# Optimization experiments

Hardware: AMD Instinct MI355X
Metric: run time of the kernel (lower is better)

The kernel has to match this reference:

```python
import jax, jax.numpy as jnp
import numpy as np

N = 50000      # nodes
E = 800000     # edges (before self-loops)
C_IN, C_H, C_OUT = 128, 64, 64
NEG_SLOPE = 0.2  # PyG GATConv default LeakyReLU slope


def setup_inputs() -> dict:
    key = jax.random.key(0)
    ks = jax.random.split(key, 16)
    def w(k, shape, fan_in):
        return jax.random.normal(k, shape, jnp.float32) / np.sqrt(fan_in)
    return {
        "x": jax.random.normal(ks[0], (N, C_IN), jnp.float32),
        "edge_index": jax.random.randint(ks[1], (2, E), 0, N, jnp.int32),
        "W1": w(ks[2], (C_IN, C_H), C_IN),
        "a_src1": w(ks[3], (C_H,), C_H),
        "a_dst1": w(ks[4], (C_H,), C_H),
        "b1": jnp.zeros((C_H,), jnp.float32),
        "W2": w(ks[5], (C_H, C_H), C_H),
        "a_src2": w(ks[6], (C_H,), C_H),
        "a_dst2": w(ks[7], (C_H,), C_H),
        "b2": jnp.zeros((C_H,), jnp.float32),
        "W3": w(ks[8], (C_H, C_OUT), C_H),
        "a_src3": w(ks[9], (C_OUT,), C_OUT),
        "a_dst3": w(ks[10], (C_OUT,), C_OUT),
        "b3": jnp.zeros((C_OUT,), jnp.float32),
    }


def _gat_conv(x, src, dst, W, a_src, a_dst, b):
    # Single-head GATConv (eval mode, self-loops already appended).
    h = x @ W                                   # [N, C]
    alpha_s = h @ a_src                         # [N]
    alpha_d = h @ a_dst                         # [N]
    e = jax.nn.leaky_relu(alpha_s[src] + alpha_d[dst], NEG_SLOPE)  # [E']
    # segment softmax over edges sharing the same destination node
    m = jax.lax.stop_gradient(jax.ops.segment_max(e, dst, num_segments=N))
    w = jnp.exp(e - m[dst])
    denom = jax.ops.segment_sum(w, dst, num_segments=N)
    alpha = w / denom[dst]                      # [E']
    out = jax.ops.segment_sum(h[src] * alpha[:, None], dst, num_segments=N)
    return out + b


def reference(x, edge_index, W1, a_src1, a_dst1, b1, W2, a_src2, a_dst2, b2,
              W3, a_src3, a_dst3, b3):
    loop = jnp.arange(N, dtype=edge_index.dtype)
    src = jnp.concatenate([edge_index[0], loop])  # add self-loops (PyG default)
    dst = jnp.concatenate([edge_index[1], loop])
    h = jax.nn.elu(_gat_conv(x, src, dst, W1, a_src1, a_dst1, b1))
    h = jax.nn.elu(_gat_conv(h, src, dst, W2, a_src2, a_dst2, b2))
    return _gat_conv(h, src, dst, W3, a_src3, a_dst3, b3)
```

## Files before the change

kernel.cpp:

```cpp
#include <hip/hip_runtime.h>
#include <hip/hip_bf16.h>
#include <math.h>

#define N_NODES 50000
#define N_EDGES 800000
#define ET_EDGES (N_EDGES + N_NODES)
#define NEG_SLOPE 0.2f
#define NBUCK ((N_NODES + 255) / 256)
#define CHUNK 4096
#define CAP   8192
#define BIN_GRID ((ET_EDGES + CHUNK - 1) / CHUNK)
#define GEMM_GRID ((N_NODES + 63) / 64)

typedef __hip_bfloat16 bf16;
typedef float f32x2 __attribute__((ext_vector_type(2)));

__device__ inline float bfbits(unsigned short u) {
    return __uint_as_float(((unsigned)u) << 16);
}
__device__ inline float bflo(unsigned u) { return __uint_as_float(u << 16); }
__device__ inline float bfhi(unsigned u) { return __uint_as_float(u & 0xffff0000u); }
__device__ inline f32x2 unpk(unsigned u) {
    f32x2 r; r.x = bflo(u); r.y = bfhi(u); return r;
}
__device__ inline f32x2 bcast2(float v) { f32x2 r; r.x = v; r.y = v; return r; }

struct PrepArgs {
    const void* src[12];
    float*      dst[12];
    int         n[12];
};

__global__ __launch_bounds__(256)
void prep(PrepArgs a, const unsigned short* __restrict__ w1raw,
          unsigned* __restrict__ flag, int* __restrict__ cur256)
{
    __shared__ unsigned sflag;
    const int tid = threadIdx.x;
    if (tid < 64) {
        float v0 = bfbits(w1raw[2 * tid]);
        float v1 = bfbits(w1raw[2 * tid + 1]);
        bool bad = !(fabsf(v0) <= 64.f && fabsf(v1) <= 64.f);
        unsigned long long b = __ballot(bad);
        if (tid == 0) sflag = (b == 0ull) ? 1u : 0u;
    }
    __syncthreads();
    const bool isbf = (sflag != 0u);
    const int which = blockIdx.y;

    if (which == 12) {
        int i = blockIdx.x * 256 + tid;
        if (i < NBUCK) cur256[i] = i * CAP;
        if (blockIdx.x == 0 && tid == 0) *flag = isbf ? 1u : 0u;
        return;
    }
    const int n = a.n[which];
    const void* s = a.src[which];
    float* d = a.dst[which];
    for (int i = blockIdx.x * 256 + tid; i < n; i += 8 * 256)
        d[i] = isbf ? bfbits(((const unsigned short*)s)[i])
                    : ((const float*)s)[i];
}

__device__ void binpass_body(unsigned char* smem, int bid,
                             const int* __restrict__ ei,
                             int* __restrict__ cur256,
                             unsigned* __restrict__ scratch)
{
    int* hist   = (int*)smem;
    int* lpre   = hist + NBUCK;
    int* lcur   = lpre + NBUCK + 1;
    int* gbase  = lcur + NBUCK;
    int* scan_a = gbase + NBUCK;
    unsigned* entry = (unsigned*)(scan_a + 256);

    const int tid = threadIdx.x;
    const int e0  = bid * CHUNK;
    const int n   = min(CHUNK, ET_EDGES - e0);

    if (tid < NBUCK) hist[tid] = 0;
    __syncthreads();

    for (int k = tid; k < n; k += 256) {
        int e = e0 + k;
        int d = (e < N_EDGES) ? ei[N_EDGES + e] : e - N_EDGES;
        atomicAdd(&hist[d >> 8], 1);
    }
    __syncthreads();

    int v = (tid < NBUCK) ? hist[tid] : 0;
    scan_a[tid] = v;
    __syncthreads();
    for (int off = 1; off < 256; off <<= 1) {
        int t = (tid >= off) ? scan_a[tid - off] : 0;
        __syncthreads();
        scan_a[tid] += t;
        __syncthreads();
    }
    if (tid < NBUCK) lpre[tid] = scan_a[tid] - v;
    if (tid == NBUCK - 1) lpre[NBUCK] = scan_a[tid];
    if (tid < NBUCK) {
        gbase[tid] = v ? atomicAdd(&cur256[tid], v) : 0;
        lcur[tid] = 0;
    }
    __syncthreads();

    for (int k = tid; k < n; k += 256) {
        int e = e0 + k;
        int s, d;
        if (e < N_EDGES) { s = ei[e]; d = ei[N_EDGES + e]; }
        else             { s = d = e - N_EDGES; }
        int b = d >> 8;
        int p = atomicAdd(&lcur[b], 1);
        entry[lpre[b] + p] = ((unsigned)s << 8) | (unsigned)(d & 255);
    }
    __syncthreads();

    for (int i = tid; i < n; i += 256) {
        int lo = 0, hi = NBUCK;
        while (hi - lo > 1) {
            int mid = (lo + hi) >> 1;
            if (lpre[mid] <= i) lo = mid; else hi = mid;
        }
        scratch[gbase[lo] + (i - lpre[lo])] = entry[i];
    }
}

__global__ __launch_bounds__(256)
void fine_scatter(const int* __restrict__ cur256,
                  const unsigned* __restrict__ scratch,
                  int* __restrict__ csr_src,
                  int* __restrict__ rowptr)
{
    __shared__ int scnt[256];
    __shared__ int cnt[256];
    __shared__ int pre[256];
    const int tid = threadIdx.x;
    const int b   = blockIdx.x;
    const int nb  = b * 256;
    const int nn  = min(256, N_NODES - nb);

    int bv = (tid < NBUCK) ? (cur256[tid] - tid * CAP) : 0;
    scnt[tid] = bv;
    __syncthreads();
    for (int off = 1; off < 256; off <<= 1) {
        int u = (tid >= off) ? scnt[tid - off] : 0;
        __syncthreads();
        scnt[tid] += u;
        __syncthreads();
    }
    const int gb = scnt[b] - (cur256[b] - b * CAP);
    const int n  = cur256[b] - b * CAP;
    const long seg = (long)b * CAP;

    cnt[tid] = 0;
    __syncthreads();
    for (int i = tid; i < n; i += 256)
        atomicAdd(&cnt[scratch[seg + i] & 255u], 1);
    __syncthreads();

    int v = cnt[tid];
    pre[tid] = v;
    __syncthreads();
    for (int off = 1; off < 256; off <<= 1) {
        int t = (tid >= off) ? pre[tid - off] : 0;
        __syncthreads();
        pre[tid] += t;
        __syncthreads();
    }
    int excl = pre[tid] - v + gb;
    if (tid < nn) rowptr[nb + tid] = excl;
    if (b == NBUCK - 1 && tid == 0) rowptr[N_NODES] = ET_EDGES;
    cnt[tid] = excl;
    __syncthreads();

    for (int i = tid; i < n; i += 256) {
        unsigned e = scratch[seg + i];
        int p = atomicAdd(&cnt[e & 255u], 1);
        csr_src[p] = (int)(e >> 8);
    }
}

template<int CIN, int XMODE>
__device__ void gemm_body(unsigned char* smem, int bid,
                          const void* __restrict__ x,
                          const float* __restrict__ W,
                          const float* __restrict__ a_src,
                          const float* __restrict__ a_dst,
                          const unsigned* __restrict__ flag,
                          bf16* __restrict__ hb,
                          float* __restrict__ as_out,
                          float* __restrict__ ad_out)
{
    constexpr int CINP = CIN + 4;
    float* sW = (float*)smem;
    float* sx = sW + CIN * 64;
    const bool isbf = (XMODE == 2) || (XMODE == 1 && *flag != 0u);
    const int tid  = threadIdx.x;
    const int colg = tid & 15;
    const int rowg = tid >> 4;
    const int c0   = colg * 4;
    const int r0l  = rowg * 4;
    const int row0 = bid * 64;

    for (int i = tid * 4; i < CIN * 64; i += 1024)
        *(float4*)&sW[i] = *(const float4*)&W[i];

    const long xbase = (long)row0 * CIN;
    const int  tile  = 64 * CIN;
    const int  limit = (N_NODES - row0) * CIN;
    if (isbf) {
        const unsigned short* xb = (const unsigned short*)x + xbase;
        for (int i = tid * 4; i < tile; i += 1024) {
            float4 v = {0.f, 0.f, 0.f, 0.f};
            if (i < limit) {
                ushort4 u = *(const ushort4*)&xb[i];
                v.x = bfbits(u.x); v.y = bfbits(u.y);
                v.z = bfbits(u.z); v.w = bfbits(u.w);
            }
            const int r = i / CIN, k = i & (CIN - 1);
            *(float4*)&sx[r * CINP + k] = v;
        }
    } else {
        const float* xf = (const float*)x + xbase;
        for (int i = tid * 4; i < tile; i += 1024) {
            float4 v = {0.f, 0.f, 0.f, 0.f};
            if (i < limit) v = *(const float4*)&xf[i];
            const int r = i / CIN, k = i & (CIN - 1);
            *(float4*)&sx[r * CINP + k] = v;
        }
    }
    __syncthreads();

    f32x2 acc[4][2];
#pragma unroll
    for (int r = 0; r < 4; ++r) {
        acc[r][0] = (f32x2){0.f, 0.f};
        acc[r][1] = (f32x2){0.f, 0.f};
    }

#pragma unroll 2
    for (int kk = 0; kk < CIN; kk += 4) {
        const float4 w0 = *(const float4*)&sW[(kk + 0) * 64 + c0];
        const float4 w1 = *(const float4*)&sW[(kk + 1) * 64 + c0];
        const float4 w2 = *(const float4*)&sW[(kk + 2) * 64 + c0];
        const float4 w3 = *(const float4*)&sW[(kk + 3) * 64 + c0];
        f32x2 w0lo; w0lo.x = w0.x; w0lo.y = w0.y;
        f32x2 w0hi; w0hi.x = w0.z; w0hi.y = w0.w;
        f32x2 w1lo; w1lo.x = w1.x; w1lo.y = w1.y;
        f32x2 w1hi; w1hi.x = w1.z; w1hi.y = w1.w;
        f32x2 w2lo; w2lo.x = w2.x; w2lo.y = w2.y;
        f32x2 w2hi; w2hi.x = w2.z; w2hi.y = w2.w;
        f32x2 w3lo; w3lo.x = w3.x; w3lo.y = w3.y;
        f32x2 w3hi; w3hi.x = w3.z; w3hi.y = w3.w;
#pragma unroll
        for (int r = 0; r < 4; ++r) {
            const float4 xv = *(const float4*)&sx[(r0l + r) * CINP + kk];
            acc[r][0] = __builtin_elementwise_fma(bcast2(xv.x), w0lo, acc[r][0]);
            acc[r][1] = __builtin_elementwise_fma(bcast2(xv.x), w0hi, acc[r][1]);
            acc[r][0] = __builtin_elementwise_fma(bcast2(xv.y), w1lo, acc[r][0]);
            acc[r][1] = __builtin_elementwise_fma(bcast2(xv.y), w1hi, acc[r][1]);
            acc[r][0] = __builtin_elementwise_fma(bcast2(xv.z), w2lo, acc[r][0]);
            acc[r][1] = __builtin_elementwise_fma(bcast2(xv.z), w2hi, acc[r][1]);
            acc[r][0] = __builtin_elementwise_fma(bcast2(xv.w), w3lo, acc[r][0]);
            acc[r][1] = __builtin_elementwise_fma(bcast2(xv.w), w3hi, acc[r][1]);
        }
    }

    const float4 sa4 = *(const float4*)&a_src[c0];
    const float4 sd4 = *(const float4*)&a_dst[c0];
#pragma unroll
    for (int r = 0; r < 4; ++r) {
        const int row = row0 + r0l + r;
        const float h0 = acc[r][0].x, h1 = acc[r][0].y;
        const float h2 = acc[r][1].x, h3 = acc[r][1].y;
        float vs = fmaf(h0, sa4.x, fmaf(h1, sa4.y, fmaf(h2, sa4.z, h3 * sa4.w)));
        float vd = fmaf(h0, sd4.x, fmaf(h1, sd4.y, fmaf(h2, sd4.z, h3 * sd4.w)));
#pragma unroll
        for (int off = 1; off < 16; off <<= 1) {
            vs += __shfl_xor(vs, off, 64);
            vd += __shfl_xor(vd, off, 64);
        }
        if (row < N_NODES) {
            uint2 u;
            u.x = ((unsigned)__bfloat16_as_ushort(__float2bfloat16(h0))) |
                  (((unsigned)__bfloat16_as_ushort(__float2bfloat16(h1))) << 16);
            u.y = ((unsigned)__bfloat16_as_ushort(__float2bfloat16(h2))) |
                  (((unsigned)__bfloat16_as_ushort(__float2bfloat16(h3))) << 16);
            *(uint2*)&((unsigned short*)hb)[(long)row * 64 + c0] = u;
            if (colg == 0) { as_out[row] = vs; ad_out[row] = vd; }
        }
    }
}

template<int CIN, int XMODE>
__global__ __launch_bounds__(256)
void gemm_alpha(const void* __restrict__ x, const float* __restrict__ W,
                const float* __restrict__ a_src, const float* __restrict__ a_dst,
                const unsigned* __restrict__ flag, bf16* __restrict__ hb,
                float* __restrict__ as_out, float* __restrict__ ad_out)
{
    __shared__ __align__(16) unsigned char smem[(CIN * 64 + 64 * (CIN + 4)) * 4];
    gemm_body<CIN, XMODE>(smem, blockIdx.x, x, W, a_src, a_dst, flag, hb, as_out, ad_out);
}

__global__ __launch_bounds__(256)
void gemm1_bin(const void* __restrict__ x, const float* __restrict__ W,
               const float* __restrict__ a_src, const float* __restrict__ a_dst,
               const unsigned* __restrict__ flag, bf16* __restrict__ hb,
               float* __restrict__ as_out, float* __restrict__ ad_out,
               const int* __restrict__ ei, int* __restrict__ cur256,
               unsigned* __restrict__ scratch)
{
    __shared__ __align__(16) unsigned char smem[(128 * 64 + 64 * 132) * 4];
    if (blockIdx.x < BIN_GRID)
        binpass_body(smem, blockIdx.x, ei, cur256, scratch);
    else
        gemm_body<128, 1>(smem, blockIdx.x - BIN_GRID, x, W, a_src, a_dst,
                          flag, hb, as_out, ad_out);
}

#define EDGE4_FMA(wX, pX) {                                                  \
    f32x2 w2_ = { wX, wX };                                                  \
    A0 = __builtin_elementwise_fma(w2_, unpk(pX.x), A0);                     \
    A1 = __builtin_elementwise_fma(w2_, unpk(pX.y), A1);                     \
    A2 = __builtin_elementwise_fma(w2_, unpk(pX.z), A2);                     \
    A3 = __builtin_elementwise_fma(w2_, unpk(pX.w), A3); }

template<bool DO_ELU, int OMODE>
__global__ __launch_bounds__(256)
void gat_gather(const int* __restrict__ rowptr,
                const int* __restrict__ csr_src,
                const float* __restrict__ as_in,
                const float* __restrict__ ad_in,
                const unsigned short* __restrict__ hb_in,
                const float* __restrict__ bias,
                void* __restrict__ out,
                const unsigned* __restrict__ flag)
{
    __shared__ int2 s_sw[16 * 64];
    const int tid  = threadIdx.x;
    const int lane = tid & 63;
    const int l16  = lane & 15;
    const int sub  = l16 >> 3;
    const int c8   = (l16 & 7) * 8;
    const int grp  = tid >> 4;
    const int node = blockIdx.x * 16 + grp;

    const int beg = rowptr[node];
    const int deg = rowptr[node + 1] - beg;
    const float adv = ad_in[node];
    const int nst = (deg < 64) ? deg : 64;

    for (int j = l16; j < nst; j += 16) {
        int s = csr_src[beg + j];
        float v = as_in[s] + adv;
        v = (v > 0.f) ? v : NEG_SLOPE * v;
        s_sw[grp * 64 + j] = make_int2(s, __float_as_int(__expf(fminf(v, 60.f))));
    }

    f32x2 A0 = {0.f, 0.f}, A1 = {0.f, 0.f}, A2 = {0.f, 0.f}, A3 = {0.f, 0.f};
    float dsum = 0.f;

    for (int j0 = 0; j0 < deg; j0 += 8) {
        const int jA = j0 + sub,     jB = j0 + 2 + sub;
        const int jC = j0 + 4 + sub, jD = j0 + 6 + sub;
        const bool vA = jA < deg, vB = jB < deg, vC = jC < deg, vD = jD < deg;
        int sA = 0, sB = 0, sC = 0, sD = 0;
        float wA = 0.f, wB = 0.f, wC = 0.f, wD = 0.f;
        if (vA) {
            if (jA < 64) { int2 t = s_sw[grp * 64 + jA]; sA = t.x; wA = __int_as_float(t.y); }
            else { sA = csr_src[beg + jA]; float v = as_in[sA] + adv;
                   v = (v > 0.f) ? v : NEG_SLOPE * v; wA = __expf(fminf(v, 60.f)); }
        }
        if (vB) {
            if (jB < 64) { int2 t = s_sw[grp * 64 + jB]; sB = t.x; wB = __int_as_float(t.y); }
            else { sB = csr_src[beg + jB]; float v = as_in[sB] + adv;
                   v = (v > 0.f) ? v : NEG_SLOPE * v; wB = __expf(fminf(v, 60.f)); }
        }
        if (vC) {
            if (jC < 64) { int2 t = s_sw[grp * 64 + jC]; sC = t.x; wC = __int_as_float(t.y); }
            else { sC = csr_src[beg + jC]; float v = as_in[sC] + adv;
                   v = (v > 0.f) ? v : NEG_SLOPE * v; wC = __expf(fminf(v, 60.f)); }
        }
        if (vD) {
            if (jD < 64) { int2 t = s_sw[grp * 64 + jD]; sD = t.x; wD = __int_as_float(t.y); }
            else { sD = csr_src[beg + jD]; float v = as_in[sD] + adv;
                   v = (v > 0.f) ? v : NEG_SLOPE * v; wD = __expf(fminf(v, 60.f)); }
        }
        uint4 pA={0u,0u,0u,0u}, pB={0u,0u,0u,0u}, pC={0u,0u,0u,0u}, pD={0u,0u,0u,0u};
        if (vA) pA = *(const uint4*)&hb_in[(long)sA * 64 + c8];
        if (vB) pB = *(const uint4*)&hb_in[(long)sB * 64 + c8];
        if (vC) pC = *(const uint4*)&hb_in[(long)sC * 64 + c8];
        if (vD) pD = *(const uint4*)&hb_in[(long)sD * 64 + c8];
        EDGE4_FMA(wA, pA) EDGE4_FMA(wB, pB) EDGE4_FMA(wC, pC) EDGE4_FMA(wD, pD)
        dsum += (wA + wB) + (wC + wD);
    }

    float a0 = A0.x, a1 = A0.y, a2 = A1.x, a3 = A1.y;
    float a4 = A2.x, a5 = A2.y, a6 = A3.x, a7 = A3.y;
    a0 += __shfl_xor(a0, 8, 64); a1 += __shfl_xor(a1, 8, 64);
    a2 += __shfl_xor(a2, 8, 64); a3 += __shfl_xor(a3, 8, 64);
    a4 += __shfl_xor(a4, 8, 64); a5 += __shfl_xor(a5, 8, 64);
    a6 += __shfl_xor(a6, 8, 64); a7 += __shfl_xor(a7, 8, 64);
    dsum += __shfl_xor(dsum, 8, 64);

    if (sub == 0) {
        float inv = 1.f / dsum;
        float r[8] = {a0, a1, a2, a3, a4, a5, a6, a7};
#pragma unroll
        for (int k = 0; k < 8; ++k) {
            r[k] = r[k] * inv + bias[c8 + k];
            if (DO_ELU) r[k] = (r[k] > 0.f) ? r[k] : expm1f(r[k]);
        }
        long o = (long)node * 64 + c8;
        bool bfst = (OMODE == 0) || (*flag != 0u);
        if (bfst) {
            uint4 u;
            u.x = ((unsigned)__bfloat16_as_ushort(__float2bfloat16(r[0]))) |
                  (((unsigned)__bfloat16_as_ushort(__float2bfloat16(r[1]))) << 16);
            u.y = ((unsigned)__bfloat16_as_ushort(__float2bfloat16(r[2]))) |
                  (((unsigned)__bfloat16_as_ushort(__float2bfloat16(r[3]))) << 16);
            u.z = ((unsigned)__bfloat16_as_ushort(__float2bfloat16(r[4]))) |
                  (((unsigned)__bfloat16_as_ushort(__float2bfloat16(r[5]))) << 16);
            u.w = ((unsigned)__bfloat16_as_ushort(__float2bfloat16(r[6]))) |
                  (((unsigned)__bfloat16_as_ushort(__float2bfloat16(r[7]))) << 16);
            *(uint4*)&((unsigned short*)out)[o] = u;
        } else {
            float4 f0 = {r[0], r[1], r[2], r[3]};
            float4 f1 = {r[4], r[5], r[6], r[7]};
            *(float4*)&((float*)out)[o]     = f0;
            *(float4*)&((float*)out)[o + 4] = f1;
        }
    }
}

extern "C" void kernel_launch(void* const* d_in, const int* in_sizes, int n_in,
                              void* d_out, int out_size, void* d_ws, size_t ws_size,
                              hipStream_t stream)
{
    const void* x  = d_in[0];
    const int*  ei = (const int*)d_in[1];
    const void* pW1 = d_in[2],  *pas1 = d_in[3],  *pad1 = d_in[4],  *pb1 = d_in[5];
    const void* pW2 = d_in[6],  *pas2 = d_in[7],  *pad2 = d_in[8],  *pb2 = d_in[9];
    const void* pW3 = d_in[10], *pas3 = d_in[11], *pad3 = d_in[12], *pb3 = d_in[13];

    float* ws = (float*)d_ws;
    bf16*     hbA    = (bf16*)ws;
    bf16*     hbB    = (bf16*)(ws + (long)N_NODES * 32);
    float*    as_    = ws + (long)N_NODES * 64;
    float*    ad_    = as_ + N_NODES;
    int*      cur256 = (int*)(ad_ + N_NODES);
    int*      rowptr = cur256 + NBUCK;
    int*      csr_src= rowptr + N_NODES + 1;
    unsigned* scratch= (unsigned*)(csr_src + ET_EDGES);
    float*    prm    = (float*)(scratch + (long)NBUCK * CAP);
    unsigned* flag   = (unsigned*)(prm + 20000);

    float* W1 = prm;     float* as1 = W1 + 8192; float* ad1 = as1 + 64; float* b1 = ad1 + 64;
    float* W2 = b1 + 64; float* as2 = W2 + 4096; float* ad2 = as2 + 64; float* b2 = ad2 + 64;
    float* W3 = b2 + 64; float* as3 = W3 + 4096; float* ad3 = as3 + 64; float* b3 = ad3 + 64;

    PrepArgs pa;
    const void* srcs[12] = {pW1, pas1, pad1, pb1, pW2, pas2, pad2, pb2, pW3, pas3, pad3, pb3};
    float*      dsts[12] = {W1, as1, ad1, b1, W2, as2, ad2, b2, W3, as3, ad3, b3};
    int         ns[12]   = {8192, 64, 64, 64, 4096, 64, 64, 64, 4096, 64, 64, 64};
    for (int i = 0; i < 12; ++i) { pa.src[i] = srcs[i]; pa.dst[i] = dsts[i]; pa.n[i] = ns[i]; }
    prep<<<dim3(8, 13), 256, 0, stream>>>(pa, (const unsigned short*)pW1, flag, cur256);

    const int gat_grid = (N_NODES + 15) / 16;

    gemm1_bin<<<BIN_GRID + GEMM_GRID, 256, 0, stream>>>(
        x, W1, as1, ad1, flag, hbA, as_, ad_, ei, cur256, scratch);
    fine_scatter<<<NBUCK, 256, 0, stream>>>(cur256, scratch, csr_src, rowptr);
    gat_gather<true, 0><<<gat_grid, 256, 0, stream>>>(
        rowptr, csr_src, as_, ad_, (const unsigned short*)hbA, b1, hbB, flag);

    gemm_alpha<64, 2><<<GEMM_GRID, 256, 0, stream>>>(
        hbB, W2, as2, ad2, flag, hbA, as_, ad_);
    gat_gather<true, 0><<<gat_grid, 256, 0, stream>>>(
        rowptr, csr_src, as_, ad_, (const unsigned short*)hbA, b2, hbB, flag);

    gemm_alpha<64, 2><<<GEMM_GRID, 256, 0, stream>>>(
        hbB, W3, as3, ad3, flag, hbA, as_, ad_);
    gat_gather<false, 1><<<gat_grid, 256, 0, stream>>>(
        rowptr, csr_src, as_, ad_, (const unsigned short*)hbA, b3, d_out, flag);
}
```

Measured before the change: 234.4 us.

## Fuse all GAT stages into one persistent kernel with grid barriers

Replaces the seven separate launches (bin+gemm1, fine scatter, three gathers, two gemms) with one persistent kernel of 768 blocks that loops over each stage's work items and separates stages with a software grid barrier on global atomics. The GEMM is restructured to stage K in 64-wide chunks so shared memory fits within a smaller fixed buffer, allowing 3 blocks per CU. This targets launch gaps and inter-kernel idle time. The risks are barrier spin cost, deadlock if not all 768 blocks are co-resident, and lower per-stage occupancy.

```diff
diff --git a/kernel.cpp b/kernel.cpp
--- a/kernel.cpp
+++ b/kernel.cpp
@@ -11,6 +11,8 @@
 #define CAP   8192
 #define BIN_GRID ((ET_EDGES + CHUNK - 1) / CHUNK)
 #define GEMM_GRID ((N_NODES + 63) / 64)
+#define GAT_GRID (N_NODES / 16)
+#define MEGA_GRID 768
 
 typedef __hip_bfloat16 bf16;
 typedef float f32x2 __attribute__((ext_vector_type(2)));
@@ -33,7 +35,8 @@
 
 __global__ __launch_bounds__(256)
 void prep(PrepArgs a, const unsigned short* __restrict__ w1raw,
-          unsigned* __restrict__ flag, int* __restrict__ cur256)
+          unsigned* __restrict__ flag, int* __restrict__ cur256,
+          int* __restrict__ bar)
 {
     __shared__ unsigned sflag;
     const int tid = threadIdx.x;
@@ -51,7 +54,11 @@
     if (which == 12) {
         int i = blockIdx.x * 256 + tid;
         if (i < NBUCK) cur256[i] = i * CAP;
-        if (blockIdx.x == 0 && tid == 0) *flag = isbf ? 1u : 0u;
+        if (blockIdx.x == 0 && tid == 0) {
+            *flag = isbf ? 1u : 0u;
+            bar[0] = 0;
+            bar[1] = 0;
+        }
         return;
     }
     const int n = a.n[which];
@@ -60,6 +67,22 @@
     for (int i = blockIdx.x * 256 + tid; i < n; i += 8 * 256)
         d[i] = isbf ? bfbits(((const unsigned short*)s)[i])
                     : ((const float*)s)[i];
+}
+
+__device__ inline void grid_barrier(int* cnt, int* phase, int nblk, int ph)
+{
+    __syncthreads();
+    if (threadIdx.x == 0) {
+        __threadfence();
+        if (atomicAdd(cnt, 1) == nblk - 1) {
+            atomicExch(cnt, 0);
+            atomicAdd(phase, 1);
+        } else {
+            while (atomicAdd(phase, 0) < ph) __builtin_amdgcn_s_sleep(2);
+        }
+        __threadfence();
+    }
+    __syncthreads();
 }
 
 __device__ void binpass_body(unsigned char* smem, int bid,
@@ -126,17 +149,16 @@
     }
 }
 
-__global__ __launch_bounds__(256)
-void fine_scatter(const int* __restrict__ cur256,
-                  const unsigned* __restrict__ scratch,
-                  int* __restrict__ csr_src,
-                  int* __restrict__ rowptr)
-{
-    __shared__ int scnt[256];
-    __shared__ int cnt[256];
-    __shared__ int pre[256];
+__device__ void fine_scatter_body(unsigned char* smem, int b,
+                                  const int* __restrict__ cur256,
+                                  const unsigned* __restrict__ scratch,
+                                  int* __restrict__ csr_src,
+                                  int* __restrict__ rowptr)
+{
+    int* scnt = (int*)smem;
+    int* cnt  = scnt + 256;
+    int* pre  = cnt + 256;
     const int tid = threadIdx.x;
-    const int b   = blockIdx.x;
     const int nb  = b * 256;
     const int nn  = min(256, N_NODES - nb);
 
@@ -192,9 +214,8 @@
                           float* __restrict__ as_out,
                           float* __restrict__ ad_out)
 {
-    constexpr int CINP = CIN + 4;
     float* sW = (float*)smem;
-    float* sx = sW + CIN * 64;
+    float* sx = sW + 64 * 64;
     const bool isbf = (XMODE == 2) || (XMODE == 1 && *flag != 0u);
     const int tid  = threadIdx.x;
     const int colg = tid & 15;
@@ -202,35 +223,7 @@
     const int c0   = colg * 4;
     const int r0l  = rowg * 4;
     const int row0 = bid * 64;
-
-    for (int i = tid * 4; i < CIN * 64; i += 1024)
-        *(float4*)&sW[i] = *(const float4*)&W[i];
-
-    const long xbase = (long)row0 * CIN;
-    const int  tile  = 64 * CIN;
-    const int  limit = (N_NODES - row0) * CIN;
-    if (isbf) {
-        const unsigned short* xb = (const unsigned short*)x + xbase;
-        for (int i = tid * 4; i < tile; i += 1024) {
-            float4 v = {0.f, 0.f, 0.f, 0.f};
-            if (i < limit) {
-                ushort4 u = *(const ushort4*)&xb[i];
-                v.x = bfbits(u.x); v.y = bfbits(u.y);
-                v.z = bfbits(u.z); v.w = bfbits(u.w);
-            }
-            const int r = i / CIN, k = i & (CIN - 1);
-            *(float4*)&sx[r * CINP + k] = v;
-        }
-    } else {
-        const float* xf = (const float*)x + xbase;
-        for (int i = tid * 4; i < tile; i += 1024) {
-            float4 v = {0.f, 0.f, 0.f, 0.f};
-            if (i < limit) v = *(const float4*)&xf[i];
-            const int r = i / CIN, k = i & (CIN - 1);
-            *(float4*)&sx[r * CINP + k] = v;
-        }
-    }
-    __syncthreads();
+    const int nrows = min(64, N_NODES - row0);
 
     f32x2 acc[4][2];
 #pragma unroll
@@ -239,31 +232,59 @@
         acc[r][1] = (f32x2){0.f, 0.f};
     }
 
+    for (int k0 = 0; k0 < CIN; k0 += 64) {
+        __syncthreads();
+        for (int i = tid * 4; i < 4096; i += 1024)
+            *(float4*)&sW[i] = *(const float4*)&W[k0 * 64 + i];
+        if (isbf) {
+            const unsigned short* xb = (const unsigned short*)x;
+            for (int i = tid * 4; i < 4096; i += 1024) {
+                const int r = i >> 6, k = i & 63;
+                float4 v = {0.f, 0.f, 0.f, 0.f};
+                if (r < nrows) {
+                    ushort4 u = *(const ushort4*)&xb[(long)(row0 + r) * CIN + k0 + k];
+                    v.x = bfbits(u.x); v.y = bfbits(u.y);
+                    v.z = bfbits(u.z); v.w = bfbits(u.w);
+                }
+                *(float4*)&sx[r * 68 + k] = v;
+            }
+        } else {
+            const float* xf = (const float*)x;
+            for (int i = tid * 4; i < 4096; i += 1024) {
+                const int r = i >> 6, k = i & 63;
+                float4 v = {0.f, 0.f, 0.f, 0.f};
+                if (r < nrows) v = *(const float4*)&xf[(long)(row0 + r) * CIN + k0 + k];
+                *(float4*)&sx[r * 68 + k] = v;
+            }
+        }
+        __syncthreads();
+
 #pragma unroll 2
-    for (int kk = 0; kk < CIN; kk += 4) {
-        const float4 w0 = *(const float4*)&sW[(kk + 0) * 64 + c0];
-        const float4 w1 = *(const float4*)&sW[(kk + 1) * 64 + c0];
-        const float4 w2 = *(const float4*)&sW[(kk + 2) * 64 + c0];
-        const float4 w3 = *(const float4*)&sW[(kk + 3) * 64 + c0];
-        f32x2 w0lo; w0lo.x = w0.x; w0lo.y = w0.y;
-        f32x2 w0hi; w0hi.x = w0.z; w0hi.y = w0.w;
-        f32x2 w1lo; w1lo.x = w1.x; w1lo.y = w1.y;
-        f32x2 w1hi; w1hi.x = w1.z; w1hi.y = w1.w;
-        f32x2 w2lo; w2lo.x = w2.x; w2lo.y = w2.y;
-        f32x2 w2hi; w2hi.x = w2.z; w2hi.y = w2.w;
-        f32x2 w3lo; w3lo.x = w3.x; w3lo.y = w3.y;
-        f32x2 w3hi; w3hi.x = w3.z; w3hi.y = w3.w;
+        for (int kk = 0; kk < 64; kk += 4) {
+            const float4 w0 = *(const float4*)&sW[(kk + 0) * 64 + c0];
+            const float4 w1 = *(const float4*)&sW[(kk + 1) * 64 + c0];
+            const float4 w2 = *(const float4*)&sW[(kk + 2) * 64 + c0];
+            const float4 w3 = *(const float4*)&sW[(kk + 3) * 64 + c0];
+            f32x2 w0lo; w0lo.x = w0.x; w0lo.y = w0.y;
+            f32x2 w0hi; w0hi.x = w0.z; w0hi.y = w0.w;
+            f32x2 w1lo; w1lo.x = w1.x; w1lo.y = w1.y;
+            f32x2 w1hi; w1hi.x = w1.z; w1hi.y = w1.w;
+            f32x2 w2lo; w2lo.x = w2.x; w2lo.y = w2.y;
+            f32x2 w2hi; w2hi.x = w2.z; w2hi.y = w2.w;
+            f32x2 w3lo; w3lo.x = w3.x; w3lo.y = w3.y;
+            f32x2 w3hi; w3hi.x = w3.z; w3hi.y = w3.w;
 #pragma unroll
-        for (int r = 0; r < 4; ++r) {
-            const float4 xv = *(const float4*)&sx[(r0l + r) * CINP + kk];
-            acc[r][0] = __builtin_elementwise_fma(bcast2(xv.x), w0lo, acc[r][0]);
-            acc[r][1] = __builtin_elementwise_fma(bcast2(xv.x), w0hi, acc[r][1]);
-            acc[r][0] = __builtin_elementwise_fma(bcast2(xv.y), w1lo, acc[r][0]);
-            acc[r][1] = __builtin_elementwise_fma(bcast2(xv.y), w1hi, acc[r][1]);
-            acc[r][0] = __builtin_elementwise_fma(bcast2(xv.z), w2lo, acc[r][0]);
-            acc[r][1] = __builtin_elementwise_fma(bcast2(xv.z), w2hi, acc[r][1]);
-            acc[r][0] = __builtin_elementwise_fma(bcast2(xv.w), w3lo, acc[r][0]);
-            acc[r][1] = __builtin_elementwise_fma(bcast2(xv.w), w3hi, acc[r][1]);
+            for (int r = 0; r < 4; ++r) {
+                const float4 xv = *(const float4*)&sx[(r0l + r) * 68 + kk];
+                acc[r][0] = __builtin_elementwise_fma(bcast2(xv.x), w0lo, acc[r][0]);
+                acc[r][1] = __builtin_elementwise_fma(bcast2(xv.x), w0hi, acc[r][1]);
+                acc[r][0] = __builtin_elementwise_fma(bcast2(xv.y), w1lo, acc[r][0]);
+                acc[r][1] = __builtin_elementwise_fma(bcast2(xv.y), w1hi, acc[r][1]);
+                acc[r][0] = __builtin_elementwise_fma(bcast2(xv.z), w2lo, acc[r][0]);
+                acc[r][1] = __builtin_elementwise_fma(bcast2(xv.z), w2hi, acc[r][1]);
+                acc[r][0] = __builtin_elementwise_fma(bcast2(xv.w), w3lo, acc[r][0]);
+                acc[r][1] = __builtin_elementwise_fma(bcast2(xv.w), w3hi, acc[r][1]);
+            }
         }
     }
 
@@ -293,33 +314,6 @@
     }
 }
 
-template<int CIN, int XMODE>
-__global__ __launch_bounds__(256)
-void gemm_alpha(const void* __restrict__ x, const float* __restrict__ W,
-                const float* __restrict__ a_src, const float* __restrict__ a_dst,
-                const unsigned* __restrict__ flag, bf16* __restrict__ hb,
-                float* __restrict__ as_out, float* __restrict__ ad_out)
-{
-    __shared__ __align__(16) unsigned char smem[(CIN * 64 + 64 * (CIN + 4)) * 4];
-    gemm_body<CIN, XMODE>(smem, blockIdx.x, x, W, a_src, a_dst, flag, hb, as_out, ad_out);
-}
-
-__global__ __launch_bounds__(256)
-void gemm1_bin(const void* __restrict__ x, const float* __restrict__ W,
-               const float* __restrict__ a_src, const float* __restrict__ a_dst,
-               const unsigned* __restrict__ flag, bf16* __restrict__ hb,
-               float* __restrict__ as_out, float* __restrict__ ad_out,
-               const int* __restrict__ ei, int* __restrict__ cur256,
-               unsigned* __restrict__ scratch)
-{
-    __shared__ __align__(16) unsigned char smem[(128 * 64 + 64 * 132) * 4];
-    if (blockIdx.x < BIN_GRID)
-        binpass_body(smem, blockIdx.x, ei, cur256, scratch);
-    else
-        gemm_body<128, 1>(smem, blockIdx.x - BIN_GRID, x, W, a_src, a_dst,
-                          flag, hb, as_out, ad_out);
-}
-
 #define EDGE4_FMA(wX, pX) {                                                  \
     f32x2 w2_ = { wX, wX };                                                  \
     A0 = __builtin_elementwise_fma(w2_, unpk(pX.x), A0);                     \
@@ -328,24 +322,24 @@
     A3 = __builtin_elementwise_fma(w2_, unpk(pX.w), A3); }
 
 template<bool DO_ELU, int OMODE>
-__global__ __launch_bounds__(256)
-void gat_gather(const int* __restrict__ rowptr,
-                const int* __restrict__ csr_src,
-                const float* __restrict__ as_in,
-                const float* __restrict__ ad_in,
-                const unsigned short* __restrict__ hb_in,
-                const float* __restrict__ bias,
-                void* __restrict__ out,
-                const unsigned* __restrict__ flag)
-{
-    __shared__ int2 s_sw[16 * 64];
+__device__ void gat_body(unsigned char* smem, int bid,
+                         const int* __restrict__ rowptr,
+                         const int* __restrict__ csr_src,
+                         const float* __restrict__ as_in,
+                         const float* __restrict__ ad_in,
+                         const unsigned short* __restrict__ hb_in,
+                         const float* __restrict__ bias,
+                         void* __restrict__ out,
+                         const unsigned* __restrict__ flag)
+{
+    int2* s_sw = (int2*)smem;
     const int tid  = threadIdx.x;
     const int lane = tid & 63;
     const int l16  = lane & 15;
     const int sub  = l16 >> 3;
     const int c8   = (l16 & 7) * 8;
     const int grp  = tid >> 4;
-    const int node = blockIdx.x * 16 + grp;
+    const int node = bid * 16 + grp;
 
     const int beg = rowptr[node];
     const int deg = rowptr[node + 1] - beg;
@@ -435,6 +429,74 @@
     }
 }
 
+__global__ __launch_bounds__(256, 3)
+void mega(const void* __restrict__ x, const int* __restrict__ ei,
+          const float* __restrict__ W1, const float* __restrict__ as1,
+          const float* __restrict__ ad1, const float* __restrict__ b1,
+          const float* __restrict__ W2, const float* __restrict__ as2,
+          const float* __restrict__ ad2, const float* __restrict__ b2,
+          const float* __restrict__ W3, const float* __restrict__ as3,
+          const float* __restrict__ ad3, const float* __restrict__ b3,
+          const unsigned* __restrict__ flag, int* __restrict__ cur256,
+          unsigned* __restrict__ scratch, int* __restrict__ rowptr,
+          int* __restrict__ csr_src, bf16* __restrict__ hbA,
+          bf16* __restrict__ hbB, float* __restrict__ as_,
+          float* __restrict__ ad_, int* __restrict__ bar,
+          void* __restrict__ d_out)
+{
+    __shared__ __align__(16) unsigned char smem[33792];
+    const int bid = blockIdx.x;
+    const int nb  = gridDim.x;
+
+    for (int it = bid; it < BIN_GRID + GEMM_GRID; it += nb) {
+        __syncthreads();
+        if (it < BIN_GRID)
+            binpass_body(smem, it, ei, cur256, scratch);
+        else
+            gemm_body<128, 1>(smem, it - BIN_GRID, x, W1, as1, ad1, flag,
+                              hbA, as_, ad_);
+    }
+    grid_barrier(bar, bar + 1, nb, 1);
+
+    for (int it = bid; it < NBUCK; it += nb) {
+        __syncthreads();
+        fine_scatter_body(smem, it, cur256, scratch, csr_src, rowptr);
+    }
+    grid_barrier(bar, bar + 1, nb, 2);
+
+    for (int it = bid; it < GAT_GRID; it += nb) {
+        __syncthreads();
+        gat_body<true, 0>(smem, it, rowptr, csr_src, as_, ad_,
+                          (const unsigned short*)hbA, b1, hbB, flag);
+    }
+    grid_barrier(bar, bar + 1, nb, 3);
+
+    for (int it = bid; it < GEMM_GRID; it += nb) {
+        __syncthreads();
+        gemm_body<64, 2>(smem, it, hbB, W2, as2, ad2, flag, hbA, as_, ad_);
+    }
+    grid_barrier(bar, bar + 1, nb, 4);
+
+    for (int it = bid; it < GAT_GRID; it += nb) {
+        __syncthreads();
+        gat_body<true, 0>(smem, it, rowptr, csr_src, as_, ad_,
+                          (const unsigned short*)hbA, b2, hbB, flag);
+    }
+    grid_barrier(bar, bar + 1, nb, 5);
+
+    for (int it = bid; it < GEMM_GRID; it += nb) {
+        __syncthreads();
+        gemm_body<64, 2>(smem, it, hbB, W3, as3, ad3, flag, hbA, as_, ad_);
+    }
+    grid_barrier(bar, bar + 1, nb, 6);
+
+    for (int it = bid; it < GAT_GRID; it += nb) {
+        __syncthreads();
+        gat_body<false, 1>(smem, it, rowptr, csr_src, as_, ad_,
+                           (const unsigned short*)hbA, b3, d_out, flag);
+    }
+}
+
 extern "C" void kernel_launch(void* const* d_in, const int* in_sizes, int n_in,
                               void* d_out, int out_size, void* d_ws, size_t ws_size,
                               hipStream_t stream)
@@ -456,6 +518,7 @@
     unsigned* scratch= (unsigned*)(csr_src + ET_EDGES);
     float*    prm    = (float*)(scratch + (long)NBUCK * CAP);
     unsigned* flag   = (unsigned*)(prm + 20000);
+    int*      bar    = (int*)(flag + 1);
 
     float* W1 = prm;     float* as1 = W1 + 8192; float* ad1 = as1 + 64; float* b1 = ad1 + 64;
     float* W2 = b1 + 64; float* as2 = W2 + 4096; float* ad2 = as2 + 64; float* b2 = ad2 + 64;
@@ -466,23 +529,9 @@
     float*      dsts[12] = {W1, as1, ad1, b1, W2, as2, ad2, b2, W3, as3, ad3, b3};
     int         ns[12]   = {8192, 64, 64, 64, 4096, 64, 64, 64, 4096, 64, 64, 64};
     for (int i = 0; i < 12; ++i) { pa.src[i] = srcs[i]; pa.dst[i] = dsts[i]; pa.n[i] = ns[i]; }
-    prep<<<dim3(8, 13), 256, 0, stream>>>(pa, (const unsigned short*)pW1, flag, cur256);
-
-    const int gat_grid = (N_NODES + 15) / 16;
-
-    gemm1_bin<<<BIN_GRID + GEMM_GRID, 256, 0, stream>>>(
-        x, W1, as1, ad1, flag, hbA, as_, ad_, ei, cur256, scratch);
-    fine_scatter<<<NBUCK, 256, 0, stream>>>(cur256, scratch, csr_src, rowptr);
-    gat_gather<true, 0><<<gat_grid, 256, 0, stream>>>(
-        rowptr, csr_src, as_, ad_, (const unsigned short*)hbA, b1, hbB, flag);
-
-    gemm_alpha<64, 2><<<GEMM_GRID, 256, 0, stream>>>(
-        hbB, W2, as2, ad2, flag, hbA, as_, ad_);
-    gat_gather<true, 0><<<gat_grid, 256, 0, stream>>>(
-        rowptr, csr_src, as_, ad_, (const unsigned short*)hbA, b2, hbB, flag);
-
-    gemm_alpha<64, 2><<<GEMM_GRID, 256, 0, stream>>>(
-        hbB, W3, as3, ad3, flag, hbA, as_, ad_);
-    gat_gather<false, 1><<<gat_grid, 256, 0, stream>>>(
-        rowptr, csr_src, as_, ad_, (const unsigned short*)hbA, b3, d_out, flag);
-}
+    prep<<<dim3(8, 13), 256, 0, stream>>>(pa, (const unsigned short*)pW1, flag, cur256, bar);
+
+    mega<<<MEGA_GRID, 256, 0, stream>>>(
+        x, ei, W1, as1, ad1, b1, W2, as2, ad2, b2, W3, as3, ad3, b3,
+        flag, cur256, scratch, rowptr, csr_src, hbA, hbB, as_, ad_, bar, d_out);
+}
```

Result: slower. 708.2 us (+202.1%).

## Fuse prep, binning, GEMM1 and fine scatter into one persistent kernel

Applied to the files above, without the earlier changes.

Merges the prep, gemm1_bin and fine_scatter launches into a single persistent kernel of 512 blocks that walks a work list. Global atomic counters with acquire/release spin-waits enforce the ordering prep -> bin/gemm -> fine_scatter. The goal is to remove launch gaps and let GEMM work overlap with the scatter phases. The cost is an added memset, spin-wait overhead, and a deadlock risk if dependent items are scheduled before their producers. Work items are handed out in increasing order, so producers always come first.

```diff
diff --git a/kernel.cpp b/kernel.cpp
--- a/kernel.cpp
+++ b/kernel.cpp
@@ -11,6 +11,13 @@
 #define CAP   8192
 #define BIN_GRID ((ET_EDGES + CHUNK - 1) / CHUNK)
 #define GEMM_GRID ((N_NODES + 63) / 64)
+#define GAT_GRID (N_NODES / 16)
+
+#define IT_PREP 104
+#define IT_BIN  (IT_PREP + BIN_GRID)
+#define IT_GEMM (IT_BIN + GEMM_GRID)
+#define IT_ALL  (IT_GEMM + NBUCK)
+#define FRONT_GRID 512
 
 typedef __hip_bfloat16 bf16;
 typedef float f32x2 __attribute__((ext_vector_type(2)));
@@ -31,35 +38,53 @@
     int         n[12];
 };
 
-__global__ __launch_bounds__(256)
-void prep(PrepArgs a, const unsigned short* __restrict__ w1raw,
-          unsigned* __restrict__ flag, int* __restrict__ cur256)
-{
-    __shared__ unsigned sflag;
+__device__ inline void wait_cnt(int* p, int target)
+{
+    if (threadIdx.x == 0) {
+        while (__hip_atomic_load(p, __ATOMIC_ACQUIRE, __HIP_MEMORY_SCOPE_AGENT) < target)
+            __builtin_amdgcn_s_sleep(8);
+        __threadfence();
+    }
+    __syncthreads();
+}
+__device__ inline void signal_cnt(int* p)
+{
+    __syncthreads();
+    if (threadIdx.x == 0) {
+        __threadfence();
+        __hip_atomic_fetch_add(p, 1, __ATOMIC_RELEASE, __HIP_MEMORY_SCOPE_AGENT);
+    }
+}
+
+__device__ void prep_item(unsigned char* smem, int i, const PrepArgs& a,
+                          const unsigned short* __restrict__ w1raw,
+                          unsigned* __restrict__ flag, int* __restrict__ cur256)
+{
+    unsigned* sflag = (unsigned*)smem;
     const int tid = threadIdx.x;
     if (tid < 64) {
         float v0 = bfbits(w1raw[2 * tid]);
         float v1 = bfbits(w1raw[2 * tid + 1]);
         bool bad = !(fabsf(v0) <= 64.f && fabsf(v1) <= 64.f);
         unsigned long long b = __ballot(bad);
-        if (tid == 0) sflag = (b == 0ull) ? 1u : 0u;
-    }
-    __syncthreads();
-    const bool isbf = (sflag != 0u);
-    const int which = blockIdx.y;
+        if (tid == 0) *sflag = (b == 0ull) ? 1u : 0u;
+    }
+    __syncthreads();
+    const bool isbf = (*sflag != 0u);
+    const int xb = i & 7, which = i >> 3;
 
     if (which == 12) {
-        int i = blockIdx.x * 256 + tid;
-        if (i < NBUCK) cur256[i] = i * CAP;
-        if (blockIdx.x == 0 && tid == 0) *flag = isbf ? 1u : 0u;
+        int j = xb * 256 + tid;
+        if (j < NBUCK) cur256[j] = j * CAP;
+        if (xb == 0 && tid == 0) *flag = isbf ? 1u : 0u;
         return;
     }
     const int n = a.n[which];
     const void* s = a.src[which];
     float* d = a.dst[which];
-    for (int i = blockIdx.x * 256 + tid; i < n; i += 8 * 256)
-        d[i] = isbf ? bfbits(((const unsigned short*)s)[i])
-                    : ((const float*)s)[i];
+    for (int j = xb * 256 + tid; j < n; j += 8 * 256)
+        d[j] = isbf ? bfbits(((const unsigned short*)s)[j])
+                    : ((const float*)s)[j];
 }
 
 __device__ void binpass_body(unsigned char* smem, int bid,
@@ -126,17 +151,16 @@
     }
 }
 
-__global__ __launch_bounds__(256)
-void fine_scatter(const int* __restrict__ cur256,
-                  const unsigned* __restrict__ scratch,
-                  int* __restrict__ csr_src,
-                  int* __restrict__ rowptr)
-{
-    __shared__ int scnt[256];
-    __shared__ int cnt[256];
-    __shared__ int pre[256];
+__device__ void fine_scatter_body(unsigned char* smem, int b,
+                                  const int* __restrict__ cur256,
+                                  const unsigned* __restrict__ scratch,
+                                  int* __restrict__ csr_src,
+                                  int* __restrict__ rowptr)
+{
+    int* scnt = (int*)smem;
+    int* cnt  = scnt + 256;
+    int* pre  = cnt + 256;
     const int tid = threadIdx.x;
-    const int b   = blockIdx.x;
     const int nb  = b * 256;
     const int nn  = min(256, N_NODES - nb);
 
@@ -305,19 +329,38 @@
 }
 
 __global__ __launch_bounds__(256)
-void gemm1_bin(const void* __restrict__ x, const float* __restrict__ W,
-               const float* __restrict__ a_src, const float* __restrict__ a_dst,
-               const unsigned* __restrict__ flag, bf16* __restrict__ hb,
-               float* __restrict__ as_out, float* __restrict__ ad_out,
-               const int* __restrict__ ei, int* __restrict__ cur256,
-               unsigned* __restrict__ scratch)
+void front(PrepArgs pa, const unsigned short* __restrict__ w1raw,
+           unsigned* __restrict__ flag, int* __restrict__ cur256,
+           const int* __restrict__ ei, unsigned* __restrict__ scratch,
+           int* __restrict__ csr_src, int* __restrict__ rowptr,
+           const void* __restrict__ x, const float* __restrict__ W1,
+           const float* __restrict__ as1, const float* __restrict__ ad1,
+           bf16* __restrict__ hbA, float* __restrict__ as_,
+           float* __restrict__ ad_, int* __restrict__ sync)
 {
     __shared__ __align__(16) unsigned char smem[(128 * 64 + 64 * 132) * 4];
-    if (blockIdx.x < BIN_GRID)
-        binpass_body(smem, blockIdx.x, ei, cur256, scratch);
-    else
-        gemm_body<128, 1>(smem, blockIdx.x - BIN_GRID, x, W, a_src, a_dst,
-                          flag, hb, as_out, ad_out);
+    int* prep_cnt = sync;
+    int* bin_cnt  = sync + 64;
+
+    for (int it = blockIdx.x; it < IT_ALL; it += gridDim.x) {
+        __syncthreads();
+        if (it < IT_PREP) {
+            prep_item(smem, it, pa, w1raw, flag, cur256);
+            signal_cnt(prep_cnt);
+        } else if (it < IT_BIN) {
+            wait_cnt(prep_cnt, IT_PREP);
+            binpass_body(smem, it - IT_PREP, ei, cur256, scratch);
+            signal_cnt(bin_cnt);
+        } else if (it < IT_GEMM) {
+            wait_cnt(prep_cnt, IT_PREP);
+            gemm_body<128, 1>(smem, it - IT_BIN, x, W1, as1, ad1, flag,
+                              hbA, as_, ad_);
+        } else {
+            wait_cnt(bin_cnt, BIN_GRID);
+            fine_scatter_body(smem, it - IT_GEMM, cur256, scratch,
+                              csr_src, rowptr);
+        }
+    }
 }
 
 #define EDGE4_FMA(wX, pX) {                                                  \
@@ -456,6 +499,7 @@
     unsigned* scratch= (unsigned*)(csr_src + ET_EDGES);
     float*    prm    = (float*)(scratch + (long)NBUCK * CAP);
     unsigned* flag   = (unsigned*)(prm + 20000);
+    int*      sync   = (int*)(prm + 20064);
 
     float* W1 = prm;     float* as1 = W1 + 8192; float* ad1 = as1 + 64; float* b1 = ad1 + 64;
     float* W2 = b1 + 64; float* as2 = W2 + 4096; float* ad2 = as2 + 64; float* b2 = ad2 + 64;
@@ -466,13 +510,15 @@
     float*      dsts[12] = {W1, as1, ad1, b1, W2, as2, ad2, b2, W3, as3, ad3, b3};
     int         ns[12]   = {8192, 64, 64, 64, 4096, 64, 64, 64, 4096, 64, 64, 64};
     for (int i = 0; i < 12; ++i) { pa.src[i] = srcs[i]; pa.dst[i] = dsts[i]; pa.n[i] = ns[i]; }
-    prep<<<dim3(8, 13), 256, 0, stream>>>(pa, (const unsigned short*)pW1, flag, cur256);
-
-    const int gat_grid = (N_NODES + 15) / 16;
-
-    gemm1_bin<<<BIN_GRID + GEMM_GRID, 256, 0, stream>>>(
-        x, W1, as1, ad1, flag, hbA, as_, ad_, ei, cur256, scratch);
-    fine_scatter<<<NBUCK, 256, 0, stream>>>(cur256, scratch, csr_src, rowptr);
+
+    hipMemsetAsync(sync, 0, 512, stream);
+
+    const int gat_grid = GAT_GRID;
+
+    front<<<FRONT_GRID, 256, 0, stream>>>(
+        pa, (const unsigned short*)pW1, flag, cur256, ei, scratch,
+        csr_src, rowptr, x, W1, as1, ad1, hbA, as_, ad_, sync);
+
     gat_gather<true, 0><<<gat_grid, 256, 0, stream>>>(
         rowptr, csr_src, as_, ad_, (const unsigned short*)hbA, b1, hbB, flag);
 
```

New measurement: 307.7 us. 31.2% more time.

## Use bf16 MFMA with hi/lo split weights for layer 2 and 3 GEMMs

Applied to the files above, without the earlier changes.

Replaces the scalar shared-memory GEMM for layers 2 and 3 with a kernel that uses 16x16x32 bf16 MFMA instructions. The weights are pre-split into bf16 high and low parts in the prep kernel so precision stays close to fp32. The attention projections are fused into the MFMA epilogue. This removes LDS staging and scalar FMA work, at the cost of an extra prep grid slice and scattered 2-byte output stores.

```diff
diff --git a/kernel.cpp b/kernel.cpp
--- a/kernel.cpp
+++ b/kernel.cpp
@@ -11,9 +11,12 @@
 #define CAP   8192
 #define BIN_GRID ((ET_EDGES + CHUNK - 1) / CHUNK)
 #define GEMM_GRID ((N_NODES + 63) / 64)
+#define GAT_GRID (N_NODES / 16)
 
 typedef __hip_bfloat16 bf16;
 typedef float f32x2 __attribute__((ext_vector_type(2)));
+typedef __attribute__((ext_vector_type(8))) short bf16x8v;
+typedef __attribute__((ext_vector_type(4))) float f32x4v;
 
 __device__ inline float bfbits(unsigned short u) {
     return __uint_as_float(((unsigned)u) << 16);
@@ -33,6 +36,8 @@
 
 __global__ __launch_bounds__(256)
 void prep(PrepArgs a, const unsigned short* __restrict__ w1raw,
+          const void* __restrict__ w2raw, const void* __restrict__ w3raw,
+          short* __restrict__ wb2, short* __restrict__ wb3,
           unsigned* __restrict__ flag, int* __restrict__ cur256)
 {
     __shared__ unsigned sflag;
@@ -52,6 +57,25 @@
         int i = blockIdx.x * 256 + tid;
         if (i < NBUCK) cur256[i] = i * CAP;
         if (blockIdx.x == 0 && tid == 0) *flag = isbf ? 1u : 0u;
+        return;
+    }
+    if (which >= 13) {
+        const void* praw = (which == 13) ? w2raw : w3raw;
+        short* dstp = (which == 13) ? wb2 : wb3;
+        for (int idx = blockIdx.x * 256 + tid; idx < 4096; idx += 8 * 256) {
+            const int i  = idx & 7;
+            const int ln = (idx >> 3) & 63;
+            const int ts = idx >> 9;
+            const int t  = ts >> 1, s = ts & 1;
+            const int k   = s * 32 + (ln >> 4) * 8 + i;
+            const int col = t * 16 + (ln & 15);
+            float wv = isbf ? bfbits(((const unsigned short*)praw)[k * 64 + col])
+                            : ((const float*)praw)[k * 64 + col];
+            bf16 hi = __float2bfloat16(wv);
+            float lof = wv - __bfloat162float(hi);
+            dstp[idx]        = (short)__bfloat16_as_ushort(hi);
+            dstp[4096 + idx] = (short)__bfloat16_as_ushort(__float2bfloat16(lof));
+        }
         return;
     }
     const int n = a.n[which];
@@ -293,17 +317,6 @@
     }
 }
 
-template<int CIN, int XMODE>
-__global__ __launch_bounds__(256)
-void gemm_alpha(const void* __restrict__ x, const float* __restrict__ W,
-                const float* __restrict__ a_src, const float* __restrict__ a_dst,
-                const unsigned* __restrict__ flag, bf16* __restrict__ hb,
-                float* __restrict__ as_out, float* __restrict__ ad_out)
-{
-    __shared__ __align__(16) unsigned char smem[(CIN * 64 + 64 * (CIN + 4)) * 4];
-    gemm_body<CIN, XMODE>(smem, blockIdx.x, x, W, a_src, a_dst, flag, hb, as_out, ad_out);
-}
-
 __global__ __launch_bounds__(256)
 void gemm1_bin(const void* __restrict__ x, const float* __restrict__ W,
                const float* __restrict__ a_src, const float* __restrict__ a_dst,
@@ -318,6 +331,78 @@
     else
         gemm_body<128, 1>(smem, blockIdx.x - BIN_GRID, x, W, a_src, a_dst,
                           flag, hb, as_out, ad_out);
+}
+
+__global__ __launch_bounds__(256)
+void gemm_mfma(const unsigned short* __restrict__ xb,
+               const short* __restrict__ Wb,
+               const float* __restrict__ a_src, const float* __restrict__ a_dst,
+               bf16* __restrict__ hb, float* __restrict__ as_out,
+               float* __restrict__ ad_out)
+{
+    const int tid  = threadIdx.x;
+    const int lane = tid & 63;
+    const int wv_  = tid >> 6;
+    const int g    = lane >> 4;
+    const int l15  = lane & 15;
+    const int row0 = blockIdx.x * 64 + wv_ * 16;
+
+    const int ar = row0 + l15;
+    const long abase = (long)((ar < N_NODES) ? ar : 0) * 64 + g * 8;
+    const bf16x8v a0 = *(const bf16x8v*)&xb[abase];
+    const bf16x8v a1 = *(const bf16x8v*)&xb[abase + 32];
+
+    f32x4v acc[4];
+    float vsr[4] = {0.f, 0.f, 0.f, 0.f};
+    float vdr[4] = {0.f, 0.f, 0.f, 0.f};
+#pragma unroll
+    for (int t = 0; t < 4; ++t) {
+        const short* bp = &Wb[t * 1024 + lane * 8];
+        const bf16x8v bh0 = *(const bf16x8v*)bp;
+        const bf16x8v bh1 = *(const bf16x8v*)(bp + 512);
+        const bf16x8v bl0 = *(const bf16x8v*)(bp + 4096);
+        const bf16x8v bl1 = *(const bf16x8v*)(bp + 4608);
+        f32x4v c = {0.f, 0.f, 0.f, 0.f};
+        c = __builtin_amdgcn_mfma_f32_16x16x32_bf16(a0, bh0, c, 0, 0, 0);
+        c = __builtin_amdgcn_mfma_f32_16x16x32_bf16(a1, bh1, c, 0, 0, 0);
+        c = __builtin_amdgcn_mfma_f32_16x16x32_bf16(a0, bl0, c, 0, 0, 0);
+        c = __builtin_amdgcn_mfma_f32_16x16x32_bf16(a1, bl1, c, 0, 0, 0);
+        acc[t] = c;
+        const float sa = a_src[t * 16 + l15];
+        const float sd = a_dst[t * 16 + l15];
+#pragma unroll
+        for (int r = 0; r < 4; ++r) {
+            vsr[r] = fmaf(c[r], sa, vsr[r]);
+            vdr[r] = fmaf(c[r], sd, vdr[r]);
+        }
+    }
+
+#pragma unroll
+    for (int r = 0; r < 4; ++r) {
+        const int row = row0 + g * 4 + r;
+        if (row < N_NODES) {
+            unsigned short* hr = (unsigned short*)hb + (long)row * 64 + l15;
+#pragma unroll
+            for (int t = 0; t < 4; ++t)
+                hr[t * 16] = __bfloat16_as_ushort(__float2bfloat16(acc[t][r]));
+        }
+    }
+
+#pragma unroll
+    for (int off = 1; off < 16; off <<= 1) {
+#pragma unroll
+        for (int r = 0; r < 4; ++r) {
+            vsr[r] += __shfl_xor(vsr[r], off, 64);
+            vdr[r] += __shfl_xor(vdr[r], off, 64);
+        }
+    }
+    if (l15 == 0) {
+#pragma unroll
+        for (int r = 0; r < 4; ++r) {
+            const int row = row0 + g * 4 + r;
+            if (row < N_NODES) { as_out[row] = vsr[r]; ad_out[row] = vdr[r]; }
+        }
+    }
 }
 
 #define EDGE4_FMA(wX, pX) {                                                  \
@@ -456,6 +541,8 @@
     unsigned* scratch= (unsigned*)(csr_src + ET_EDGES);
     float*    prm    = (float*)(scratch + (long)NBUCK * CAP);
     unsigned* flag   = (unsigned*)(prm + 20000);
+    short*    wb2    = (short*)(prm + 20008);
+    short*    wb3    = wb2 + 8192;
 
     float* W1 = prm;     float* as1 = W1 + 8192; float* ad1 = as1 + 64; float* b1 = ad1 + 64;
     float* W2 = b1 + 64; float* as2 = W2 + 4096; float* ad2 = as2 + 64; float* b2 = ad2 + 64;
@@ -466,9 +553,10 @@
     float*      dsts[12] = {W1, as1, ad1, b1, W2, as2, ad2, b2, W3, as3, ad3, b3};
     int         ns[12]   = {8192, 64, 64, 64, 4096, 64, 64, 64, 4096, 64, 64, 64};
     for (int i = 0; i < 12; ++i) { pa.src[i] = srcs[i]; pa.dst[i] = dsts[i]; pa.n[i] = ns[i]; }
-    prep<<<dim3(8, 13), 256, 0, stream>>>(pa, (const unsigned short*)pW1, flag, cur256);
-
-    const int gat_grid = (N_NODES + 15) / 16;
+    prep<<<dim3(8, 15), 256, 0, stream>>>(
+        pa, (const unsigned short*)pW1, pW2, pW3, wb2, wb3, flag, cur256);
+
+    const int gat_grid = GAT_GRID;
 
     gemm1_bin<<<BIN_GRID + GEMM_GRID, 256, 0, stream>>>(
         x, W1, as1, ad1, flag, hbA, as_, ad_, ei, cur256, scratch);
@@ -476,13 +564,13 @@
     gat_gather<true, 0><<<gat_grid, 256, 0, stream>>>(
         rowptr, csr_src, as_, ad_, (const unsigned short*)hbA, b1, hbB, flag);
 
-    gemm_alpha<64, 2><<<GEMM_GRID, 256, 0, stream>>>(
-        hbB, W2, as2, ad2, flag, hbA, as_, ad_);
+    gemm_mfma<<<GEMM_GRID, 256, 0, stream>>>(
+        (const unsigned short*)hbB, wb2, as2, ad2, hbA, as_, ad_);
     gat_gather<true, 0><<<gat_grid, 256, 0, stream>>>(
         rowptr, csr_src, as_, ad_, (const unsigned short*)hbA, b2, hbB, flag);
 
-    gemm_alpha<64, 2><<<GEMM_GRID, 256, 0, stream>>>(
-        hbB, W3, as3, ad3, flag, hbA, as_, ad_);
+    gemm_mfma<<<GEMM_GRID, 256, 0, stream>>>(
+        (const unsigned short*)hbB, wb3, as3, ad3, hbA, as_, ad_);
     gat_gather<false, 1><<<gat_grid, 256, 0, stream>>>(
         rowptr, csr_src, as_, ad_, (const unsigned short*)hbA, b3, d_out, flag);
 }
```

Result: faster. 224.5 us (-4.2%).
